# Kernel tuning notes

Hardware: AMD Instinct MI355X
Metric: run time of the kernel (lower is better)

## Reference

```python
import jax, jax.numpy as jnp
import numpy as np

V, N = 3, 32768
C2, C3 = 256, 32          # feat_ch_2D, feat_ch_3D
H = W = 128               # 2D feature map size
D = 32                    # 3D volume feature size
CIN = C2 + C3             # 288, MLP in_channels


def setup_inputs() -> dict:
    key = jax.random.key(0)
    ks = jax.random.split(key, 16)
    sc = 0.02
    inp = {
        'pts': jax.random.uniform(ks[0], (1, N, 3), minval=-0.5, maxval=0.5),
        'pts_proj': jax.random.uniform(ks[1], (1, N, 2), minval=-1.0, maxval=1.0),
        'img_feat0': jax.random.normal(ks[2], (V, C2, H, W)),
        'img_feat1': jax.random.normal(ks[3], (V, C2, H, W)),
        'vol_feat0': jax.random.normal(ks[4], (V, C3, D, D, D)),
        'vol_feat1': jax.random.normal(ks[5], (V, C3, D, D, D)),
        'W0': jax.random.normal(ks[6], (1024, CIN)) * sc,  'b0': jnp.zeros((1024,)),
        'W1': jax.random.normal(ks[7], (512, CIN + 1024)) * sc, 'b1': jnp.zeros((512,)),
        'W2': jax.random.normal(ks[8], (256, CIN + 512)) * sc,  'b2': jnp.zeros((256,)),
        'W3': jax.random.normal(ks[9], (128, CIN + 256)) * sc,  'b3': jnp.zeros((128,)),
        'W4': jax.random.normal(ks[10], (1, 128)) * sc,         'b4': jnp.zeros((1,)),
        'mean_num': 3,
    }
    return inp


def _gs2d(feat, gx, gy):
    # feat: [C,H,W]; gx,gy: [N] normalized coords in [-1,1]
    C, Hh, Ww = feat.shape
    ix = jnp.clip(((gx + 1.0) * Ww - 1.0) * 0.5, 0.0, Ww - 1.0)  # align_corners=False, border pad
    iy = jnp.clip(((gy + 1.0) * Hh - 1.0) * 0.5, 0.0, Hh - 1.0)
    x0f, y0f = jnp.floor(ix), jnp.floor(iy)
    wx, wy = ix - x0f, iy - y0f
    x0 = x0f.astype(jnp.int32); x1 = jnp.minimum(x0 + 1, Ww - 1)
    y0 = y0f.astype(jnp.int32); y1 = jnp.minimum(y0 + 1, Hh - 1)
    v00 = feat[:, y0, x0]; v01 = feat[:, y0, x1]
    v10 = feat[:, y1, x0]; v11 = feat[:, y1, x1]
    return (v00 * (1 - wy) * (1 - wx) + v01 * (1 - wy) * wx
            + v10 * wy * (1 - wx) + v11 * wy * wx)  # [C,N]


def _gs3d(feat, gx, gy, gz):
    # feat: [C,D,H,W]; grid x->W, y->H, z->D (torch grid_sample convention)
    C, Dd, Hh, Ww = feat.shape
    ix = jnp.clip(((gx + 1.0) * Ww - 1.0) * 0.5, 0.0, Ww - 1.0)
    iy = jnp.clip(((gy + 1.0) * Hh - 1.0) * 0.5, 0.0, Hh - 1.0)
    iz = jnp.clip(((gz + 1.0) * Dd - 1.0) * 0.5, 0.0, Dd - 1.0)
    x0f, y0f, z0f = jnp.floor(ix), jnp.floor(iy), jnp.floor(iz)
    wx, wy, wz = ix - x0f, iy - y0f, iz - z0f
    x0 = x0f.astype(jnp.int32); x1 = jnp.minimum(x0 + 1, Ww - 1)
    y0 = y0f.astype(jnp.int32); y1 = jnp.minimum(y0 + 1, Hh - 1)
    z0 = z0f.astype(jnp.int32); z1 = jnp.minimum(z0 + 1, Dd - 1)
    def g(zi, yi, xi):
        return feat[:, zi, yi, xi]  # [C,N]
    out = (g(z0, y0, x0) * (1 - wz) * (1 - wy) * (1 - wx)
           + g(z0, y0, x1) * (1 - wz) * (1 - wy) * wx
           + g(z0, y1, x0) * (1 - wz) * wy * (1 - wx)
           + g(z0, y1, x1) * (1 - wz) * wy * wx
           + g(z1, y0, x0) * wz * (1 - wy) * (1 - wx)
           + g(z1, y0, x1) * wz * (1 - wy) * wx
           + g(z1, y1, x0) * wz * wy * (1 - wx)
           + g(z1, y1, x1) * wz * wy * wx)
    return out  # [C,N]


def _lrelu(x):
    return jnp.where(x >= 0, x, 0.2 * x)


def _conv1x1(Wm, bm, x):
    # x: [V,C,N] -> [V,O,N]
    return jnp.einsum('oc,vcn->von', Wm, x) + bm[None, :, None]


def _mlp0(x, W0, b0, W1, b1, W2, b2, W3, b3):
    out = _lrelu(_conv1x1(W0, b0, x))
    out = _lrelu(_conv1x1(W1, b1, jnp.concatenate([x, out], axis=1)))
    out = _lrelu(_conv1x1(W2, b2, jnp.concatenate([x, out], axis=1)))
    out = _lrelu(_conv1x1(W3, b3, jnp.concatenate([x, out], axis=1)))
    return out  # [V,128,N]


def _forward(pts, pts_proj, img_feats, vol_feats,
             W0, b0, W1, b1, W2, b2, W3, b3, W4, b4, mean_num):
    v = img_feats[0].shape[0]
    gx2 = jnp.broadcast_to(pts_proj[:, :, 0], (v, pts_proj.shape[1]))
    gy2 = jnp.broadcast_to(pts_proj[:, :, 1], (v, pts_proj.shape[1]))
    p = pts * 2.0  # pts *= 2.0 before 3D sampling
    gx3 = jnp.broadcast_to(p[:, :, 0], (v, p.shape[1]))
    gy3 = jnp.broadcast_to(p[:, :, 1], (v, p.shape[1]))
    gz3 = jnp.broadcast_to(p[:, :, 2], (v, p.shape[1]))
    outs = []
    for img_feat, vol_feat in zip(img_feats, vol_feats):
        f2 = jax.vmap(_gs2d)(img_feat, gx2, gy2)            # [V,C2,N]
        f3 = jax.vmap(_gs3d)(vol_feat, gx3, gy3, gz3)       # [V,C3,N]
        pt_feat = jnp.concatenate([f2, f3], axis=1)         # [V,288,N]
        pt_out0 = _mlp0(pt_feat, W0, b0, W1, b1, W2, b2, W3, b3)
        pt_out0_mean = jnp.mean(pt_out0[:mean_num], axis=0, keepdims=True)  # [1,128,N]
        sdf = jax.nn.sigmoid(_conv1x1(W4, b4, pt_out0_mean))                # [1,1,N]
        outs.append(jnp.transpose(sdf, (0, 2, 1)))                          # [1,N,1]
    return tuple(outs)


def reference(pts, pts_proj, img_feat0, img_feat1, vol_feat0, vol_feat1,
              W0, b0, W1, b1, W2, b2, W3, b3, W4, b4, mean_num):
    return _forward(pts, pts_proj, [img_feat0, img_feat1], [vol_feat0, vol_feat1],
                    W0, b0, W1, b1, W2, b2, W3, b3, W4, b4, mean_num)
```

## Files before the change

### kernel.cpp

```cpp
#include <hip/hip_runtime.h>
#include <hip/hip_bf16.h>

#define NV 3
#define NPTS 32768
#define C2C 256
#define C3C 32
#define CINC 288
#define CINP 320
#define HH 128
#define WWW 128
#define DDD 32

typedef short bh8 __attribute__((ext_vector_type(8)));
typedef float fx4 __attribute__((ext_vector_type(4)));
typedef unsigned short us4 __attribute__((ext_vector_type(4)));

__device__ __forceinline__ float b2f(unsigned short u) {
    unsigned int x = ((unsigned int)u) << 16;
    return __uint_as_float(x);
}
__device__ __forceinline__ unsigned short f2b(float f) {
    unsigned int x = __float_as_uint(f);
    unsigned int r = (x + 0x7FFFu + ((x >> 16) & 1u)) >> 16;
    return (unsigned short)r;
}

__device__ __forceinline__ void gl2lds16(const unsigned short* g, unsigned short* l) {
    __builtin_amdgcn_global_load_lds(
        (const __attribute__((address_space(1))) unsigned int*)g,
        (__attribute__((address_space(3))) unsigned int*)l, 16, 0, 0);
}

template <int MB>
__device__ __forceinline__ void pair_decode(int b, int& mIdx, int& nIdx) {
    constexpr int L = (MB == 1) ? 0 : (MB == 2) ? 1 : 2;
    nIdx = ((b >> (3 + L)) << 3) | (b & 7);
    mIdx = (b >> 3) & (MB - 1);
}

__global__ __launch_bounds__(256) void k_prep(
    const float* __restrict__ s0, const float* __restrict__ s1,
    const float* __restrict__ s2, const float* __restrict__ s3,
    unsigned short* __restrict__ d0, unsigned short* __restrict__ d1,
    unsigned short* __restrict__ d2, unsigned short* __restrict__ d3,
    const float* __restrict__ img0, const float* __restrict__ img1,
    unsigned short* __restrict__ imgT, size_t imgStride,
    const float* __restrict__ vol0, const float* __restrict__ vol1,
    unsigned short* __restrict__ volT, size_t volStride) {
    __shared__ float smem[32 * 257];
    int b = blockIdx.x;
    if (b < 5088) {
        int base, M, Kp;
        const float* src;
        unsigned short* dst;
        if (b < 1280)      { base = 0;    M = 1024; Kp = 320;  src = s0; dst = d0; }
        else if (b < 3968) { base = 1280; M = 512;  Kp = 1344; src = s1; dst = d1; }
        else if (b < 4800) { base = 3968; M = 256;  Kp = 832;  src = s2; dst = d2; }
        else               { base = 4800; M = 128;  Kp = 576;  src = s3; dst = d3; }
        int idx = (b - base) * 256 + threadIdx.x;
        if (idx >= M * Kp) return;
        int m = idx / Kp, k = idx - m * Kp;
        int Ksrc = Kp - 32;
        float v;
        if (k < CINC) v = src[(size_t)m * Ksrc + k];
        else if (k < CINP) v = 0.0f;
        else v = src[(size_t)m * Ksrc + (k - 32)];
        dst[idx] = f2b(v);
    } else if (b < 11232) {
        int id = b - 5088;
        int bx = id % 384, by = (id / 384) & 1, bz = id / 768;
        int lvl = bz >> 2, cb = bz & 3;
        const float* in = lvl ? img1 : img0;
        int v = bx >> 7, y = bx & 127;
        int x0 = by << 6, c0 = cb << 6;
        float (*t)[65] = (float(*)[65])smem;
        int tx = threadIdx.x & 63, tg = threadIdx.x >> 6;
        const float* src = in + (((size_t)(v * C2C + c0) * HH + y) * WWW + x0);
#pragma unroll
        for (int i = 0; i < 16; i++) {
            int cl = tg * 16 + i;
            t[cl][tx] = src[(size_t)cl * (HH * WWW) + tx];
        }
        __syncthreads();
        unsigned short* dst = imgT + lvl * imgStride + ((size_t)(v * HH + y) * WWW + x0) * C2C + c0;
#pragma unroll
        for (int i = 0; i < 16; i++) {
            int xl = tg * 16 + i;
            dst[(size_t)xl * C2C + tx] = f2b(t[tx][xl]);
        }
    } else {
        int id = b - 11232;
        int v = id % 3, sy = (id / 3) & 127, lvl = id / 384;
        const float* in = lvl ? vol1 : vol0;
        int s0i = sy << 8;
        float (*t)[257] = (float(*)[257])smem;
        int tid = threadIdx.x;
        const float* src = in + (size_t)v * C3C * 32768 + s0i;
#pragma unroll
        for (int c = 0; c < 32; c++) t[c][tid] = src[(size_t)c * 32768 + tid];
        __syncthreads();
        unsigned short* dst = volT + lvl * volStride + ((size_t)v * 32768 + s0i) * C3C;
        int c = tid & 31, sb = tid >> 5;
#pragma unroll
        for (int j = 0; j < 32; j++) {
            int sl = j * 8 + sb;
            dst[(size_t)sl * C3C + c] = f2b(t[c][sl]);
        }
    }
}

__device__ __forceinline__ void sample_body(const float* __restrict__ pts, const float* __restrict__ proj,
                         const unsigned short* __restrict__ imgT, const unsigned short* __restrict__ volT,
                         unsigned short* __restrict__ ptT, int n0, int Nk) {
    int w = threadIdx.x >> 6, l = threadIdx.x & 63;
    int i = blockIdx.x * 4 + w;
    int v = blockIdx.y;
    int n = n0 + i;
    unsigned short* dstRow = ptT + (size_t)(v * Nk + i) * CINP;

    {
        float gx = proj[n * 2 + 0], gy = proj[n * 2 + 1];
        float ix = fminf(fmaxf(((gx + 1.0f) * (float)WWW - 1.0f) * 0.5f, 0.0f), (float)(WWW - 1));
        float iy = fminf(fmaxf(((gy + 1.0f) * (float)HH - 1.0f) * 0.5f, 0.0f), (float)(HH - 1));
        float x0f = floorf(ix), y0f = floorf(iy);
        float wx = ix - x0f, wy = iy - y0f;
        int x0 = (int)x0f, y0 = (int)y0f;
        int x1 = min(x0 + 1, WWW - 1), y1 = min(y0 + 1, HH - 1);
        const unsigned short* base = imgT + (size_t)v * HH * WWW * C2C;
        us4 a = *((const us4*)(base + ((size_t)(y0 * WWW + x0)) * C2C) + l);
        us4 b = *((const us4*)(base + ((size_t)(y0 * WWW + x1)) * C2C) + l);
        us4 c = *((const us4*)(base + ((size_t)(y1 * WWW + x0)) * C2C) + l);
        us4 d = *((const us4*)(base + ((size_t)(y1 * WWW + x1)) * C2C) + l);
        float w00 = (1.0f - wy) * (1.0f - wx), w01 = (1.0f - wy) * wx;
        float w10 = wy * (1.0f - wx), w11 = wy * wx;
        us4 rv;
#pragma unroll
        for (int r = 0; r < 4; r++) {
            float f = b2f(a[r]) * w00 + b2f(b[r]) * w01 + b2f(c[r]) * w10 + b2f(d[r]) * w11;
            rv[r] = f2b(f);
        }
        *(us4*)(dstRow + l * 4) = rv;
    }
    {
        float gx = pts[n * 3 + 0] * 2.0f, gy = pts[n * 3 + 1] * 2.0f, gz = pts[n * 3 + 2] * 2.0f;
        float ix = fminf(fmaxf(((gx + 1.0f) * (float)DDD - 1.0f) * 0.5f, 0.0f), (float)(DDD - 1));
        float iy = fminf(fmaxf(((gy + 1.0f) * (float)DDD - 1.0f) * 0.5f, 0.0f), (float)(DDD - 1));
        float iz = fminf(fmaxf(((gz + 1.0f) * (float)DDD - 1.0f) * 0.5f, 0.0f), (float)(DDD - 1));
        float x0f = floorf(ix), y0f = floorf(iy), z0f = floorf(iz);
        float wx = ix - x0f, wy = iy - y0f, wz = iz - z0f;
        int x0 = (int)x0f, y0 = (int)y0f, z0 = (int)z0f;
        int x1 = min(x0 + 1, DDD - 1), y1 = min(y0 + 1, DDD - 1), z1 = min(z0 + 1, DDD - 1);
        int c = l & 31, zs = l >> 5;
        int zi = zs ? z1 : z0;
        float wzs = zs ? wz : (1.0f - wz);
        const unsigned short* base = volT + (size_t)v * 32768 * C3C;
        float f00 = b2f(base[((size_t)((zi * 32 + y0) * 32 + x0)) * C3C + c]);
        float f01 = b2f(base[((size_t)((zi * 32 + y0) * 32 + x1)) * C3C + c]);
        float f10 = b2f(base[((size_t)((zi * 32 + y1) * 32 + x0)) * C3C + c]);
        float f11 = b2f(base[((size_t)((zi * 32 + y1) * 32 + x1)) * C3C + c]);
        float r = (f00 * (1.0f - wy) * (1.0f - wx) + f01 * (1.0f - wy) * wx +
                   f10 * wy * (1.0f - wx) + f11 * wy * wx) * wzs;
        float other = __shfl_xor(r, 32);
        r += other;
        if (zs == 0) dstRow[C2C + c] = f2b(r);
    }
    if (l < 8) *(us4*)(dstRow + CINC + l * 4) = (us4){0, 0, 0, 0};
}

__global__ __launch_bounds__(256) void k_sampleL0(const float* p, const float* pr, const unsigned short* im,
                                                  const unsigned short* vo, unsigned short* pt, int n0, int Nk) {
    sample_body(p, pr, im, vo, pt, n0, Nk);
}
__global__ __launch_bounds__(256) void k_sampleL1(const float* p, const float* pr, const unsigned short* im,
                                                  const unsigned short* vo, unsigned short* pt, int n0, int Nk) {
    sample_body(p, pr, im, vo, pt, n0, Nk);
}

template <int K2>
__device__ __forceinline__ void g3dot_body(const unsigned short* __restrict__ A,
                                           const unsigned short* __restrict__ B1,
                                           const unsigned short* __restrict__ B2,
                                           const float* __restrict__ bias,
                                           const float* __restrict__ W4v,
                                           float* __restrict__ dout) {
    constexpr int K1 = CINP;
    constexpr int K = K1 + K2;
    constexpr int nt1 = K1 / 32;
    constexpr int nt = K / 32;
    __shared__ unsigned short Ash[3][128 * 32];
    __shared__ unsigned short Bsh[3][128 * 32];
    __shared__ float ds[128];
    int tid = threadIdx.x;
    int w = tid >> 6, l = tid & 63;
    int la = l & 15, lg = l >> 4;
    int wm = w & 1, wn = w >> 1;
    int nBlk = blockIdx.x * 128;
    int sRow = l >> 2, sCol = (l & 3) * 8;
    int r0 = w * 32 + sRow, r1 = r0 + 16;

    const unsigned short* Ag = A;
    const unsigned short* B1g = B1 + (size_t)nBlk * K1;
    const unsigned short* B2g = B2 + (size_t)nBlk * K2;

    fx4 acc[4][4];
#pragma unroll
    for (int mi = 0; mi < 4; mi++)
#pragma unroll
        for (int ni = 0; ni < 4; ni++) acc[mi][ni] = (fx4){0.f, 0.f, 0.f, 0.f};

    auto stage = [&](int t, int b) {
        const unsigned short* as = Ag + t * 32 + sCol;
        gl2lds16(as + (size_t)r0 * K, &Ash[b][r0 * 32 + sCol]);
        gl2lds16(as + (size_t)r1 * K, &Ash[b][r1 * 32 + sCol]);
        const unsigned short* bs;
        size_t ldb;
        if (t < nt1) { bs = B1g + t * 32 + sCol; ldb = (size_t)K1; }
        else         { bs = B2g + (t - nt1) * 32 + sCol; ldb = (size_t)K2; }
        gl2lds16(bs + (size_t)r0 * ldb, &Bsh[b][r0 * 32 + sCol]);
        gl2lds16(bs + (size_t)r1 * ldb, &Bsh[b][r1 * 32 + sCol]);
    };

    stage(0, 0);
    if (nt > 1) stage(1, 1);
    asm volatile("s_waitcnt vmcnt(4)" ::: "memory");
    __builtin_amdgcn_s_barrier();
    int cur = 0, nxt2 = 2;
    for (int t = 0; t < nt; t++) {
        if (t + 2 < nt) stage(t + 2, nxt2);
        bh8 af[4], bfv[4];
#pragma unroll
        for (int mi = 0; mi < 4; mi++) af[mi] = *(const bh8*)&Ash[cur][(wm * 64 + mi * 16 + la) * 32 + lg * 8];
#pragma unroll
        for (int ni = 0; ni < 4; ni++) bfv[ni] = *(const bh8*)&Bsh[cur][(wn * 64 + ni * 16 + la) * 32 + lg * 8];
#pragma unroll
        for (int mi = 0; mi < 4; mi++)
#pragma unroll
            for (int ni = 0; ni < 4; ni++)
                acc[mi][ni] = __builtin_amdgcn_mfma_f32_16x16x32_bf16(af[mi], bfv[ni], acc[mi][ni], 0, 0, 0);
        asm volatile("s_waitcnt lgkmcnt(0)" ::: "memory");
        if (t + 2 < nt)      asm volatile("s_waitcnt vmcnt(4)" ::: "memory");
        else if (t + 1 < nt) asm volatile("s_waitcnt vmcnt(0)" ::: "memory");
        __builtin_amdgcn_s_barrier();
        cur = (cur == 2) ? 0 : cur + 1;
        nxt2 = (nxt2 == 2) ? 0 : nxt2 + 1;
    }

    if (tid < 128) ds[tid] = 0.0f;
    __syncthreads();
#pragma unroll
    for (int ni = 0; ni < 4; ni++) {
        float part = 0.0f;
#pragma unroll
        for (int mi = 0; mi < 4; mi++) {
            int m0 = wm * 64 + mi * 16 + lg * 4;
            fx4 bb = *(const fx4*)(bias + m0);
#pragma unroll
            for (int r = 0; r < 4; r++) {
                float x = acc[mi][ni][r] + bb[r];
                x = (x >= 0.0f) ? x : 0.2f * x;
                part += W4v[m0 + r] * x;
            }
        }
        part += __shfl_xor(part, 16);
        part += __shfl_xor(part, 32);
        if (lg == 0) atomicAdd(&ds[wn * 64 + ni * 16 + la], part);
    }
    __syncthreads();
    if (tid < 128) dout[nBlk + tid] = ds[tid];
}

__global__ __launch_bounds__(256) void k_g3L0(const unsigned short* A, const unsigned short* B1, const unsigned short* B2,
                                              const float* b, const float* W4, float* dout) { g3dot_body<256>(A, B1, B2, b, W4, dout); }
__global__ __launch_bounds__(256) void k_g3L1(const unsigned short* A, const unsigned short* B1, const unsigned short* B2,
                                              const float* b, const float* W4, float* dout) { g3dot_body<256>(A, B1, B2, b, W4, dout); }

template <int KP, int K2, int M, int MB>
__device__ __forceinline__ void g1t_body(const unsigned short* __restrict__ A,
                                         const unsigned short* __restrict__ B1,
                                         const unsigned short* __restrict__ B2,
                                         const float* __restrict__ bias,
                                         unsigned short* __restrict__ C) {
    constexpr int nt = KP >> 6;
    __shared__ unsigned short As[2][256 * 64];
    __shared__ unsigned short Bs[2][256 * 64];
    int tid = threadIdx.x;
    int w = tid >> 6, l = tid & 63;
    int la = l & 15, lg = l >> 4;
    int wm = w >> 2, wn = w & 3;
    int mIdx, nIdx;
    pair_decode<MB>(blockIdx.x, mIdx, nIdx);
    int mBlk = mIdx * 256;
    int nBlk = nIdx * 256;

    const unsigned short* Ag = A + (size_t)mBlk * KP;

    fx4 acc[8][4];
#pragma unroll
    for (int mi = 0; mi < 8; mi++)
#pragma unroll
        for (int ni = 0; ni < 4; ni++) acc[mi][ni] = (fx4){0.f, 0.f, 0.f, 0.f};

    auto stageB = [&](int t, int nxt) {
        const unsigned short* bsrc;
        size_t ldb;
        int kc;
        if (t < 5) { bsrc = B1; ldb = CINP; kc = t * 64; }
        else       { bsrc = B2; ldb = (size_t)K2; kc = (t - 5) * 64; }
        bsrc += (size_t)nBlk * ldb + kc;
#pragma unroll
        for (int h = 0; h < 2; h++)
#pragma unroll
            for (int j = 0; j < 2; j++) {
                int idx = j * 512 + tid;
                int r = (h << 7) + (idx >> 3);
                int c = (idx & 7) ^ (r & 7);
                gl2lds16(bsrc + (size_t)r * ldb + c * 8, &Bs[nxt][(h << 13) + idx * 8]);
            }
    };
    auto stageA1 = [&](int t, int nxt) {
        const unsigned short* asrc = Ag + t * 64;
#pragma unroll
        for (int h = 0; h < 2; h++) {
            int idx = tid;
            int r = (h << 7) + (idx >> 3);
            int c = (idx & 7) ^ (r & 7);
            gl2lds16(asrc + (size_t)r * KP + c * 8, &As[nxt][(h << 13) + idx * 8]);
        }
    };
    auto stageA2 = [&](int t, int nxt) {
        const unsigned short* asrc = Ag + t * 64;
#pragma unroll
        for (int h = 0; h < 2; h++) {
            int idx = 512 + tid;
            int r = (h << 7) + (idx >> 3);
            int c = (idx & 7) ^ (r & 7);
            gl2lds16(asrc + (size_t)r * KP + c * 8, &As[nxt][(h << 13) + idx * 8]);
        }
    };

    stageB(0, 0);
    stageA1(0, 0);
    stageA2(0, 0);
    asm volatile("s_waitcnt vmcnt(0)" ::: "memory");
    __builtin_amdgcn_s_barrier();

    for (int t = 0; t < nt; t++) {
        int cur = t & 1;
        const unsigned short* Ab = &As[cur][0];
        const unsigned short* Bb = &Bs[cur][0];
        bh8 afr[4][2];
#pragma unroll
        for (int p = 0; p < 4; p++) {
            int qm = p >> 1, qn = p & 1;
            if (qn == 0) {
#pragma unroll
                for (int m2 = 0; m2 < 4; m2++)
#pragma unroll
                    for (int s = 0; s < 2; s++) {
                        int row = wm * 128 + (qm * 4 + m2) * 16 + la;
                        int c = (s * 4 + lg) ^ (row & 7);
                        afr[m2][s] = *(const bh8*)&Ab[row * 64 + c * 8];
                    }
            }
            bh8 bfr[2][2];
#pragma unroll
            for (int n2 = 0; n2 < 2; n2++)
#pragma unroll
                for (int s = 0; s < 2; s++) {
                    int row = wn * 64 + (qn * 2 + n2) * 16 + la;
                    int c = (s * 4 + lg) ^ (row & 7);
                    bfr[n2][s] = *(const bh8*)&Bb[row * 64 + c * 8];
                }
            if (p == 0 && t + 1 < nt) stageB(t + 1, cur ^ 1);
            if (p == 1 && t + 1 < nt) stageA1(t + 1, cur ^ 1);
            if (p == 2 && t + 1 < nt) stageA2(t + 1, cur ^ 1);
            __builtin_amdgcn_s_barrier();
            __builtin_amdgcn_s_setprio(1);
#pragma unroll
            for (int m2 = 0; m2 < 4; m2++)
#pragma unroll
                for (int n2 = 0; n2 < 2; n2++)
#pragma unroll
                    for (int s = 0; s < 2; s++)
                        acc[qm * 4 + m2][qn * 2 + n2] = __builtin_amdgcn_mfma_f32_16x16x32_bf16(
                            afr[m2][s], bfr[n2][s], acc[qm * 4 + m2][qn * 2 + n2], 0, 0, 0);
            __builtin_amdgcn_s_setprio(0);
            if (p == 1) {
                if (t + 1 < nt) asm volatile("s_waitcnt vmcnt(6)" ::: "memory");
                else            asm volatile("s_waitcnt vmcnt(0)" ::: "memory");
            }
            if (p == 3) {
                asm volatile("s_waitcnt lgkmcnt(0)" ::: "memory");
                if (t + 1 < nt) asm volatile("s_waitcnt vmcnt(2)" ::: "memory");
            }
            __builtin_amdgcn_s_barrier();
        }
    }

#pragma unroll
    for (int mi = 0; mi < 8; mi++) {
        int m0 = mBlk + wm * 128 + mi * 16 + lg * 4;
        fx4 bb = *(const fx4*)(bias + m0);
#pragma unroll
        for (int ni = 0; ni < 4; ni++) {
            int n = nBlk + wn * 64 + ni * 16 + la;
            us4 rv;
#pragma unroll
            for (int r = 0; r < 4; r++) {
                float x = acc[mi][ni][r] + bb[r];
                x = (x >= 0.0f) ? x : 0.2f * x;
                rv[r] = f2b(x);
            }
            *(us4*)(C + (size_t)n * M + m0) = rv;
        }
    }
}

__global__ __launch_bounds__(512) void k_g0L0(const unsigned short* A, const unsigned short* B1,
                                              const float* b, unsigned short* C) { g1t_body<320, 0, 1024, 4>(A, B1, nullptr, b, C); }
__global__ __launch_bounds__(512) void k_g0L1(const unsigned short* A, const unsigned short* B1,
                                              const float* b, unsigned short* C) { g1t_body<320, 0, 1024, 4>(A, B1, nullptr, b, C); }
__global__ __launch_bounds__(512) void k_g1L0(const unsigned short* A, const unsigned short* B1, const unsigned short* B2,
                                              const float* b, unsigned short* C) { g1t_body<1344, 1024, 512, 2>(A, B1, B2, b, C); }
__global__ __launch_bounds__(512) void k_g1L1(const unsigned short* A, const unsigned short* B1, const unsigned short* B2,
                                              const float* b, unsigned short* C) { g1t_body<1344, 1024, 512, 2>(A, B1, B2, b, C); }
__global__ __launch_bounds__(512) void k_g2L0(const unsigned short* A, const unsigned short* B1, const unsigned short* B2,
                                              const float* b, unsigned short* C) { g1t_body<832, 512, 256, 1>(A, B1, B2, b, C); }
__global__ __launch_bounds__(512) void k_g2L1(const unsigned short* A, const unsigned short* B1, const unsigned short* B2,
                                              const float* b, unsigned short* C) { g1t_body<832, 512, 256, 1>(A, B1, B2, b, C); }

__global__ __launch_bounds__(256) void k_fin(const float* __restrict__ d, const float* __restrict__ b4,
                                             const int* __restrict__ mn_p, float* __restrict__ out,
                                             int n0, int Nk, int level) {
    int i = blockIdx.x * 256 + threadIdx.x;
    if (i >= Nk) return;
    int mn = *mn_p;
    if (mn > NV) mn = NV;
    if (mn < 1) mn = 1;
    float s = 0.0f;
    for (int v = 0; v < mn; v++) s += d[(size_t)v * Nk + i];
    s = s / (float)mn + b4[0];
    out[(size_t)level * NPTS + n0 + i] = 1.0f / (1.0f + expf(-s));
}

extern "C" void kernel_launch(void* const* d_in, const int* in_sizes, int n_in,
                              void* d_out, int out_size, void* d_ws, size_t ws_size,
                              hipStream_t stream) {
    const float* pts = (const float*)d_in[0];
    const float* proj = (const float*)d_in[1];
    const float* img[2] = {(const float*)d_in[2], (const float*)d_in[3]};
    const float* vol[2] = {(const float*)d_in[4], (const float*)d_in[5]};
    const float* Wf[4] = {(const float*)d_in[6], (const float*)d_in[8], (const float*)d_in[10], (const float*)d_in[12]};
    const float* bf[4] = {(const float*)d_in[7], (const float*)d_in[9], (const float*)d_in[11], (const float*)d_in[13]};
    const float* W4 = (const float*)d_in[14];
    const float* b4 = (const float*)d_in[15];
    const int* mn = (const int*)d_in[16];
    float* out = (float*)d_out;

    const int Kp[4] = {320, 1344, 832, 576};
    const int Msz[4] = {1024, 512, 256, 128};

    char* ws = (char*)d_ws;
    size_t off = 0;
    auto alloc = [&](size_t bytes) -> char* {
        char* p = ws + off;
        off = (off + bytes + 255) & ~(size_t)255;
        return p;
    };

    const size_t imgStride = (size_t)NV * HH * WWW * C2C;
    const size_t volStride = (size_t)NV * 32768 * C3C;

    unsigned short* Wb[4];
    for (int i = 0; i < 4; i++) Wb[i] = (unsigned short*)alloc((size_t)Msz[i] * Kp[i] * 2);
    unsigned short* imgT = (unsigned short*)alloc(2 * imgStride * 2);
    unsigned short* volT = (unsigned short*)alloc(2 * volStride * 2);
    size_t fixed = off;

    const size_t perPt = (size_t)NV * (2 * (CINP + 1024 + 512) + 4);
    int Nk = NPTS;
    if (fixed + (size_t)Nk * perPt + 4096 > ws_size) {
        size_t avail = (ws_size > fixed + 4096) ? (ws_size - fixed - 4096) : 0;
        long nk = (long)(avail / perPt);
        nk = (nk / 2048) * 2048;
        if (nk < 2048) nk = 2048;
        if (nk > NPTS) nk = NPTS;
        Nk = (int)nk;
    }
    unsigned short* ptT = (unsigned short*)alloc((size_t)NV * Nk * CINP * 2);
    unsigned short* o0 = (unsigned short*)alloc((size_t)NV * Nk * 1024 * 2);
    unsigned short* o1 = (unsigned short*)alloc((size_t)NV * Nk * 512 * 2);
    unsigned short* o2 = o0;
    float* dsum = (float*)alloc((size_t)NV * Nk * 4);

    k_prep<<<12000, 256, 0, stream>>>(Wf[0], Wf[1], Wf[2], Wf[3], Wb[0], Wb[1], Wb[2], Wb[3],
                                      img[0], img[1], imgT, imgStride, vol[0], vol[1], volT, volStride);

    for (int n0 = 0; n0 < NPTS; n0 += Nk) {
        int nk = NPTS - n0 < Nk ? NPTS - n0 : Nk;
        int NC = NV * nk;
        int nP256 = NC / 256;
        int nP128 = NC / 128;
        k_sampleL0<<<dim3(nk / 4, NV), 256, 0, stream>>>(pts, proj, imgT, volT, ptT, n0, nk);
        k_g0L0<<<4 * nP256, 512, 0, stream>>>(Wb[0], ptT, bf[0], o0);
        k_g1L0<<<2 * nP256, 512, 0, stream>>>(Wb[1], ptT, o0, bf[1], o1);
        k_g2L0<<<1 * nP256, 512, 0, stream>>>(Wb[2], ptT, o1, bf[2], o2);
        k_g3L0<<<nP128, 256, 0, stream>>>(Wb[3], ptT, o2, bf[3], W4, dsum);
        k_fin<<<(nk + 255) / 256, 256, 0, stream>>>(dsum, b4, mn, out, n0, nk, 0);
        k_sampleL1<<<dim3(nk / 4, NV), 256, 0, stream>>>(pts, proj, imgT + imgStride, volT + volStride, ptT, n0, nk);
        k_g0L1<<<4 * nP256, 512, 0, stream>>>(Wb[0], ptT, bf[0], o0);
        k_g1L1<<<2 * nP256, 512, 0, stream>>>(Wb[1], ptT, o0, bf[1], o1);
        k_g2L1<<<1 * nP256, 512, 0, stream>>>(Wb[2], ptT, o1, bf[2], o2);
        k_g3L1<<<nP128, 256, 0, stream>>>(Wb[3], ptT, o2, bf[3], W4, dsum);
        k_fin<<<(nk + 255) / 256, 256, 0, stream>>>(dsum, b4, mn, out, n0, nk, 1);
    }
}
```

Before: 1.027 ms.

## Add single-buffered swizzled GEMM for layer 2 and merge final sigmoid launches

Replaces the generic GEMM body for the third MLP layer (M=256) with a dedicated kernel. It stages 256x64 A and B tiles into swizzled LDS, uses a 2x4 wave grid with 16x16x32 bf16 MFMA, and raises wave priority around the MFMA bursts. It also splits the per-level partial sums into two buffers so one 2D-grid final kernel computes both levels' sigmoid outputs, dropping one launch per chunk. The new GEMM is single-buffered with a full vmcnt wait each K step, so global loads are not overlapped with compute.

```diff
diff --git a/kernel.cpp b/kernel.cpp
--- a/kernel.cpp
+++ b/kernel.cpp
@@ -416,6 +416,110 @@
     }
 }
 
+template <int KP, int K2, int M>
+__device__ __forceinline__ void g2sb_body(const unsigned short* __restrict__ A,
+                                          const unsigned short* __restrict__ B1,
+                                          const unsigned short* __restrict__ B2,
+                                          const float* __restrict__ bias,
+                                          unsigned short* __restrict__ C) {
+    constexpr int nt = KP >> 6;
+    __shared__ unsigned short As[256 * 64];
+    __shared__ unsigned short Bs[256 * 64];
+    int tid = threadIdx.x;
+    int w = tid >> 6, l = tid & 63;
+    int la = l & 15, lg = l >> 4;
+    int wm = w >> 2, wn = w & 3;
+    int nBlk = blockIdx.x * 256;
+
+    const unsigned short* Ag = A;
+
+    fx4 acc[8][4];
+#pragma unroll
+    for (int mi = 0; mi < 8; mi++)
+#pragma unroll
+        for (int ni = 0; ni < 4; ni++) acc[mi][ni] = (fx4){0.f, 0.f, 0.f, 0.f};
+
+    auto stage = [&](int t) {
+        const unsigned short* bsrc;
+        size_t ldb;
+        int kc;
+        if (t < 5) { bsrc = B1; ldb = CINP; kc = t * 64; }
+        else       { bsrc = B2; ldb = (size_t)K2; kc = (t - 5) * 64; }
+        bsrc += (size_t)nBlk * ldb + kc;
+        const unsigned short* asrc = Ag + t * 64;
+#pragma unroll
+        for (int h = 0; h < 2; h++)
+#pragma unroll
+            for (int j = 0; j < 2; j++) {
+                int idx = j * 512 + tid;
+                int r = (h << 7) + (idx >> 3);
+                int c = (idx & 7) ^ (r & 7);
+                gl2lds16(asrc + (size_t)r * KP + c * 8, &As[(h << 13) + idx * 8]);
+                gl2lds16(bsrc + (size_t)r * ldb + c * 8, &Bs[(h << 13) + idx * 8]);
+            }
+    };
+
+    for (int t = 0; t < nt; t++) {
+        stage(t);
+        asm volatile("s_waitcnt vmcnt(0)" ::: "memory");
+        __builtin_amdgcn_s_barrier();
+        bh8 afr[4][2];
+#pragma unroll
+        for (int p = 0; p < 4; p++) {
+            int qm = p >> 1, qn = p & 1;
+            if (qn == 0) {
+#pragma unroll
+                for (int m2 = 0; m2 < 4; m2++)
+#pragma unroll
+                    for (int s = 0; s < 2; s++) {
+                        int row = wm * 128 + (qm * 4 + m2) * 16 + la;
+                        int c = (s * 4 + lg) ^ (row & 7);
+                        afr[m2][s] = *(const bh8*)&As[row * 64 + c * 8];
+                    }
+            }
+            bh8 bfr[2][2];
+#pragma unroll
+            for (int n2 = 0; n2 < 2; n2++)
+#pragma unroll
+                for (int s = 0; s < 2; s++) {
+                    int row = wn * 64 + (qn * 2 + n2) * 16 + la;
+                    int c = (s * 4 + lg) ^ (row & 7);
+                    bfr[n2][s] = *(const bh8*)&Bs[row * 64 + c * 8];
+                }
+            __builtin_amdgcn_s_setprio(1);
+#pragma unroll
+            for (int m2 = 0; m2 < 4; m2++)
+#pragma unroll
+                for (int n2 = 0; n2 < 2; n2++)
+#pragma unroll
+                    for (int s = 0; s < 2; s++)
+                        acc[qm * 4 + m2][qn * 2 + n2] = __builtin_amdgcn_mfma_f32_16x16x32_bf16(
+                            afr[m2][s], bfr[n2][s], acc[qm * 4 + m2][qn * 2 + n2], 0, 0, 0);
+            __builtin_amdgcn_s_setprio(0);
+        }
+        asm volatile("s_waitcnt lgkmcnt(0)" ::: "memory");
+        __builtin_amdgcn_s_barrier();
+    }
+
+#pragma unroll
+    for (int mi = 0; mi < 8; mi++) {
+        int m0 = wm * 128 + mi * 16 + lg * 4;
+        fx4 bb = *(const fx4*)(bias + m0);
+#pragma unroll
+        for (int ni = 0; ni < 4; ni++) {
+            int n = nBlk + wn * 64 + ni * 16 + la;
+            us4 rv;
+#pragma unroll
+            for (int r = 0; r < 4; r++) {
+                float x = acc[mi][ni][r] + bb[r];
+                x = (x >= 0.0f) ? x : 0.2f * x;
+                rv[r] = f2b(x);
+            }
+            *(us4*)(C + (size_t)n * M + m0) = rv;
+        }
+    }
+}
+
 __global__ __launch_bounds__(512) void k_g0L0(const unsigned short* A, const unsigned short* B1,
                                               const float* b, unsigned short* C) { g1t_body<320, 0, 1024, 4>(A, B1, nullptr, b, C); }
 __global__ __launch_bounds__(512) void k_g0L1(const unsigned short* A, const unsigned short* B1,
@@ -425,22 +529,24 @@
 __global__ __launch_bounds__(512) void k_g1L1(const unsigned short* A, const unsigned short* B1, const unsigned short* B2,
                                               const float* b, unsigned short* C) { g1t_body<1344, 1024, 512, 2>(A, B1, B2, b, C); }
 __global__ __launch_bounds__(512) void k_g2L0(const unsigned short* A, const unsigned short* B1, const unsigned short* B2,
-                                              const float* b, unsigned short* C) { g1t_body<832, 512, 256, 1>(A, B1, B2, b, C); }
+                                              const float* b, unsigned short* C) { g2sb_body<832, 512, 256>(A, B1, B2, b, C); }
 __global__ __launch_bounds__(512) void k_g2L1(const unsigned short* A, const unsigned short* B1, const unsigned short* B2,
-                                              const float* b, unsigned short* C) { g1t_body<832, 512, 256, 1>(A, B1, B2, b, C); }
-
-__global__ __launch_bounds__(256) void k_fin(const float* __restrict__ d, const float* __restrict__ b4,
-                                             const int* __restrict__ mn_p, float* __restrict__ out,
-                                             int n0, int Nk, int level) {
+                                              const float* b, unsigned short* C) { g2sb_body<832, 512, 256>(A, B1, B2, b, C); }
+
+__global__ __launch_bounds__(256) void k_fin2(const float* __restrict__ d0v, const float* __restrict__ d1v,
+                                              const float* __restrict__ b4, const int* __restrict__ mn_p,
+                                              float* __restrict__ out, int n0, int Nk) {
     int i = blockIdx.x * 256 + threadIdx.x;
+    int lvl = blockIdx.y;
     if (i >= Nk) return;
+    const float* d = lvl ? d1v : d0v;
     int mn = *mn_p;
     if (mn > NV) mn = NV;
     if (mn < 1) mn = 1;
     float s = 0.0f;
     for (int v = 0; v < mn; v++) s += d[(size_t)v * Nk + i];
     s = s / (float)mn + b4[0];
-    out[(size_t)level * NPTS + n0 + i] = 1.0f / (1.0f + expf(-s));
+    out[(size_t)lvl * NPTS + n0 + i] = 1.0f / (1.0f + expf(-s));
 }
 
 extern "C" void kernel_launch(void* const* d_in, const int* in_sizes, int n_in,
@@ -477,7 +583,7 @@
     unsigned short* volT = (unsigned short*)alloc(2 * volStride * 2);
     size_t fixed = off;
 
-    const size_t perPt = (size_t)NV * (2 * (CINP + 1024 + 512) + 4);
+    const size_t perPt = (size_t)NV * (2 * (CINP + 1024 + 512) + 8);
     int Nk = NPTS;
     if (fixed + (size_t)Nk * perPt + 4096 > ws_size) {
         size_t avail = (ws_size > fixed + 4096) ? (ws_size - fixed - 4096) : 0;
@@ -491,7 +597,8 @@
     unsigned short* o0 = (unsigned short*)alloc((size_t)NV * Nk * 1024 * 2);
     unsigned short* o1 = (unsigned short*)alloc((size_t)NV * Nk * 512 * 2);
     unsigned short* o2 = o0;
-    float* dsum = (float*)alloc((size_t)NV * Nk * 4);
+    float* dsum0 = (float*)alloc((size_t)NV * Nk * 4);
+    float* dsum1 = (float*)alloc((size_t)NV * Nk * 4);
 
     k_prep<<<12000, 256, 0, stream>>>(Wf[0], Wf[1], Wf[2], Wf[3], Wb[0], Wb[1], Wb[2], Wb[3],
                                       img[0], img[1], imgT, imgStride, vol[0], vol[1], volT, volStride);
@@ -504,14 +611,13 @@
         k_sampleL0<<<dim3(nk / 4, NV), 256, 0, stream>>>(pts, proj, imgT, volT, ptT, n0, nk);
         k_g0L0<<<4 * nP256, 512, 0, stream>>>(Wb[0], ptT, bf[0], o0);
         k_g1L0<<<2 * nP256, 512, 0, stream>>>(Wb[1], ptT, o0, bf[1], o1);
-        k_g2L0<<<1 * nP256, 512, 0, stream>>>(Wb[2], ptT, o1, bf[2], o2);
-        k_g3L0<<<nP128, 256, 0, stream>>>(Wb[3], ptT, o2, bf[3], W4, dsum);
-        k_fin<<<(nk + 255) / 256, 256, 0, stream>>>(dsum, b4, mn, out, n0, nk, 0);
+        k_g2L0<<<nP256, 512, 0, stream>>>(Wb[2], ptT, o1, bf[2], o2);
+        k_g3L0<<<nP128, 256, 0, stream>>>(Wb[3], ptT, o2, bf[3], W4, dsum0);
         k_sampleL1<<<dim3(nk / 4, NV), 256, 0, stream>>>(pts, proj, imgT + imgStride, volT + volStride, ptT, n0, nk);
         k_g0L1<<<4 * nP256, 512, 0, stream>>>(Wb[0], ptT, bf[0], o0);
         k_g1L1<<<2 * nP256, 512, 0, stream>>>(Wb[1], ptT, o0, bf[1], o1);
-        k_g2L1<<<1 * nP256, 512, 0, stream>>>(Wb[2], ptT, o1, bf[2], o2);
-        k_g3L1<<<nP128, 256, 0, stream>>>(Wb[3], ptT, o2, bf[3], W4, dsum);
-        k_fin<<<(nk + 255) / 256, 256, 0, stream>>>(dsum, b4, mn, out, n0, nk, 1);
-    }
-}
+        k_g2L1<<<nP256, 512, 0, stream>>>(Wb[2], ptT, o1, bf[2], o2);
+        k_g3L1<<<nP128, 256, 0, stream>>>(Wb[3], ptT, o2, bf[3], W4, dsum1);
+        k_fin2<<<dim3((nk + 255) / 256, 2), 256, 0, stream>>>(dsum0, dsum1, b4, mn, out, n0, nk);
+    }
+}
```

New measurement: 1.003 ms (median of 2 runs). 2.3% less time.
